# Kernel optimization log

Hardware: AMD Instinct MI355X
Metric: run time of the kernel (lower is better)

## Reference

```python
import jax, jax.numpy as jnp
import numpy as np

N, C = 262144, 128
BN_EPS = 1e-5


def setup_inputs() -> dict:
    key = jax.random.key(0)
    ks = jax.random.split(key, 9)
    s = 1.0 / np.sqrt(C)  # torch Linear default init scale
    return {
        "x": jax.random.normal(ks[0], (N, C), dtype=jnp.float32),
        "W1": jax.random.uniform(ks[1], (C, C), jnp.float32, -s, s),
        "b1": jax.random.uniform(ks[2], (C,), jnp.float32, -s, s),
        "gamma1": jnp.ones((C,), jnp.float32),
        "beta1": jnp.zeros((C,), jnp.float32),
        "W2": jax.random.uniform(ks[3], (C, C), jnp.float32, -s, s),
        "b2": jax.random.uniform(ks[4], (C,), jnp.float32, -s, s),
        "gamma2": jnp.ones((C,), jnp.float32),
        "beta2": jnp.zeros((C,), jnp.float32),
    }


def _batchnorm(h, gamma, beta):
    # training-mode BatchNorm1d: batch mean, biased variance, eps=1e-5
    m = jnp.mean(h, axis=0)
    v = jnp.var(h, axis=0)
    return (h - m) * jax.lax.rsqrt(v + BN_EPS) * gamma + beta


def reference(x, W1, b1, gamma1, beta1, W2, b2, gamma2, beta2):
    res = x
    out = x @ W1.T + b1
    # contextNormalization: only the in-place `d -= mean` loop has effect
    # (return value is discarded in the original), i.e. mean-center over batch
    out = out - jnp.mean(out, axis=0)
    out = jax.nn.relu(_batchnorm(out, gamma1, beta1))
    out = out @ W2.T + b2
    out = out - jnp.mean(out, axis=0)
    out = jax.nn.relu(_batchnorm(out, gamma2, beta2))
    return out + res
```

## Files before the change

### kernel.cpp

```cpp
#include <hip/hip_runtime.h>
#include <hip/hip_bf16.h>

#define NROWS 262144
#define CDIM  128
#define BN_EPS 1e-5f
#define GGRID 1024
#define SPB   (NROWS / 16 / GGRID)

typedef __attribute__((ext_vector_type(8))) short bf16x8;
typedef __attribute__((ext_vector_type(4))) float f32x4;
#define LROW 136

static __device__ __forceinline__ unsigned int f2bf_rtn(float f) {
  unsigned int u = __float_as_uint(f);
  return (u + 0x7fffu + ((u >> 16) & 1u)) >> 16;
}
static __device__ __forceinline__ float bf2f(unsigned int b) {
  return __uint_as_float(b << 16);
}

template <bool NORM>
__global__ void __launch_bounds__(256, 4)
gemm_bn(const float* __restrict__ in, const float* __restrict__ W,
        const float* __restrict__ bias, const float* __restrict__ scsh,
        float* __restrict__ hout, float* __restrict__ stats)
{
  __shared__ __align__(16) short lds[2][2][16][LROW];

  const int tid  = threadIdx.x;
  const int lane = tid & 63;
  const int wave = tid >> 6;
  const int l15  = lane & 15;
  const int lq   = lane >> 4;
  const int wcol = wave * 32;
  const int srow = tid >> 4;
  const int sk0  = (tid & 15) * 8;

  bf16x8 bh[2][4], bl[2][4];
#pragma unroll
  for (int jt = 0; jt < 2; ++jt) {
    const float* wrow = W + (wcol + jt * 16 + l15) * CDIM;
#pragma unroll
    for (int ks = 0; ks < 4; ++ks) {
      const int k0 = ks * 32 + lq * 8;
      f32x4 w0 = *(const f32x4*)(wrow + k0);
      f32x4 w1 = *(const f32x4*)(wrow + k0 + 4);
      float wv[8] = {w0.x,w0.y,w0.z,w0.w,w1.x,w1.y,w1.z,w1.w};
#pragma unroll
      for (int e = 0; e < 8; ++e) {
        unsigned int h = f2bf_rtn(wv[e]);
        bh[jt][ks][e] = (short)h;
        bl[jt][ks][e] = (short)f2bf_rtn(wv[e] - bf2f(h));
      }
    }
  }

  float scv[8], shv[8];
  if constexpr (NORM) {
#pragma unroll
    for (int e = 0; e < 8; ++e) {
      scv[e] = scsh[sk0 + e];
      shv[e] = scsh[CDIM + sk0 + e];
    }
  }

  const float bias0 = bias[wcol + l15];
  const float bias1 = bias[wcol + 16 + l15];
  float s0 = 0.f, s1 = 0.f, q0 = 0.f, q1 = 0.f;

  const int row0 = blockIdx.x * (SPB * 16);

  auto cvt_write = [&](int buf, f32x4 g0, f32x4 g1) {
    float av[8] = {g0.x,g0.y,g0.z,g0.w,g1.x,g1.y,g1.z,g1.w};
    if constexpr (NORM) {
#pragma unroll
      for (int e = 0; e < 8; ++e)
        av[e] = fmaxf(av[e] * scv[e] + shv[e], 0.f);
    }
    bf16x8 hi, lo;
#pragma unroll
    for (int e = 0; e < 8; ++e) {
      unsigned int h = f2bf_rtn(av[e]);
      hi[e] = (short)h;
      lo[e] = (short)f2bf_rtn(av[e] - bf2f(h));
    }
    *(bf16x8*)&lds[buf][0][srow][sk0] = hi;
    *(bf16x8*)&lds[buf][1][srow][sk0] = lo;
  };

  {
    const float* ap = in + (size_t)(row0 + srow) * CDIM + sk0;
    f32x4 g0 = *(const f32x4*)ap;
    f32x4 g1 = *(const f32x4*)(ap + 4);
    cvt_write(0, g0, g1);
  }
  __syncthreads();

  for (int s = 0; s < SPB; ++s) {
    const int cur = s & 1;
    const int r0 = row0 + s * 16;

    f32x4 g0 = {0,0,0,0}, g1 = {0,0,0,0};
    const bool more = (s + 1 < SPB);
    if (more) {
      const float* ap = in + (size_t)(r0 + 16 + srow) * CDIM + sk0;
      g0 = *(const f32x4*)ap;
      g1 = *(const f32x4*)(ap + 4);
    }

    f32x4 acc0 = {0.f,0.f,0.f,0.f};
    f32x4 acc1 = {0.f,0.f,0.f,0.f};
#pragma unroll
    for (int ks = 0; ks < 4; ++ks) {
      const int kc = ks * 32 + lq * 8;
      bf16x8 ah = *(const bf16x8*)&lds[cur][0][l15][kc];
      bf16x8 al = *(const bf16x8*)&lds[cur][1][l15][kc];
      acc0 = __builtin_amdgcn_mfma_f32_16x16x32_bf16(al, bh[0][ks], acc0, 0, 0, 0);
      acc0 = __builtin_amdgcn_mfma_f32_16x16x32_bf16(ah, bl[0][ks], acc0, 0, 0, 0);
      acc0 = __builtin_amdgcn_mfma_f32_16x16x32_bf16(ah, bh[0][ks], acc0, 0, 0, 0);
      acc1 = __builtin_amdgcn_mfma_f32_16x16x32_bf16(al, bh[1][ks], acc1, 0, 0, 0);
      acc1 = __builtin_amdgcn_mfma_f32_16x16x32_bf16(ah, bl[1][ks], acc1, 0, 0, 0);
      acc1 = __builtin_amdgcn_mfma_f32_16x16x32_bf16(ah, bh[1][ks], acc1, 0, 0, 0);
    }

    if (more) cvt_write(cur ^ 1, g0, g1);
    __syncthreads();

    float* op = hout + (size_t)(r0 + lq * 4) * CDIM + wcol + l15;
#pragma unroll
    for (int r = 0; r < 4; ++r) {
      float h0 = acc0[r] + bias0;
      float h1 = acc1[r] + bias1;
      s0 += h0; q0 += h0 * h0;
      s1 += h1; q1 += h1 * h1;
      op[r * CDIM] = h0;
      op[r * CDIM + 16] = h1;
    }
  }

  s0 += __shfl_xor(s0, 16); s0 += __shfl_xor(s0, 32);
  s1 += __shfl_xor(s1, 16); s1 += __shfl_xor(s1, 32);
  q0 += __shfl_xor(q0, 16); q0 += __shfl_xor(q0, 32);
  q1 += __shfl_xor(q1, 16); q1 += __shfl_xor(q1, 32);
  if (lane < 16) {
    atomicAdd(&stats[wcol + lane],             s0);
    atomicAdd(&stats[wcol + 16 + lane],        s1);
    atomicAdd(&stats[CDIM + wcol + lane],      q0);
    atomicAdd(&stats[CDIM + wcol + 16 + lane], q1);
  }
}

__global__ void __launch_bounds__(128)
bn_coeffs(const float* __restrict__ stats, const float* __restrict__ gamma,
          const float* __restrict__ beta, float* __restrict__ scsh)
{
  const int c = threadIdx.x;
  const float inv_n = 1.0f / (float)NROWS;
  float m  = stats[c] * inv_n;
  float v  = stats[CDIM + c] * inv_n - m * m;
  float sc = gamma[c] * rsqrtf(v + BN_EPS);
  scsh[c]        = sc;
  scsh[CDIM + c] = beta[c] - m * sc;
}

__global__ void __launch_bounds__(256)
finalize(const f32x4* __restrict__ h2, const f32x4* __restrict__ xin,
         const float* __restrict__ scsh, f32x4* __restrict__ outp)
{
  const int n4 = NROWS * CDIM / 4;
  const int stride = gridDim.x * blockDim.x * 2;
  for (int i = (blockIdx.x * blockDim.x + threadIdx.x) * 2; i < n4; i += stride) {
    f32x4 hA = h2[i], hB = h2[i + 1];
    f32x4 xA = xin[i], xB = xin[i + 1];
    const int c0 = (i << 2) & (CDIM - 1);
    f32x4 scA = *(const f32x4*)(scsh + c0);
    f32x4 scB = *(const f32x4*)(scsh + c0 + 4);
    f32x4 shA = *(const f32x4*)(scsh + CDIM + c0);
    f32x4 shB = *(const f32x4*)(scsh + CDIM + c0 + 4);
    f32x4 oA, oB;
    oA.x = fmaxf(hA.x * scA.x + shA.x, 0.f) + xA.x;
    oA.y = fmaxf(hA.y * scA.y + shA.y, 0.f) + xA.y;
    oA.z = fmaxf(hA.z * scA.z + shA.z, 0.f) + xA.z;
    oA.w = fmaxf(hA.w * scA.w + shA.w, 0.f) + xA.w;
    oB.x = fmaxf(hB.x * scB.x + shB.x, 0.f) + xB.x;
    oB.y = fmaxf(hB.y * scB.y + shB.y, 0.f) + xB.y;
    oB.z = fmaxf(hB.z * scB.z + shB.z, 0.f) + xB.z;
    oB.w = fmaxf(hB.w * scB.w + shB.w, 0.f) + xB.w;
    __builtin_nontemporal_store(oA, &outp[i]);
    __builtin_nontemporal_store(oB, &outp[i + 1]);
  }
}

extern "C" void kernel_launch(void* const* d_in, const int* in_sizes, int n_in,
                              void* d_out, int out_size, void* d_ws, size_t ws_size,
                              hipStream_t stream) {
  (void)in_sizes; (void)n_in; (void)out_size; (void)ws_size;
  const float* x   = (const float*)d_in[0];
  const float* W1  = (const float*)d_in[1];
  const float* b1  = (const float*)d_in[2];
  const float* g1  = (const float*)d_in[3];
  const float* be1 = (const float*)d_in[4];
  const float* W2  = (const float*)d_in[5];
  const float* b2  = (const float*)d_in[6];
  const float* g2  = (const float*)d_in[7];
  const float* be2 = (const float*)d_in[8];

  float* hbuf   = (float*)d_out;
  float* stats1 = (float*)d_ws;
  float* stats2 = stats1 + 256;
  float* scsh1  = stats1 + 512;
  float* scsh2  = stats1 + 768;

  (void)hipMemsetAsync(d_ws, 0, 2048, stream);

  gemm_bn<false><<<GGRID, 256, 0, stream>>>(x, W1, b1, nullptr, hbuf, stats1);
  bn_coeffs<<<1, 128, 0, stream>>>(stats1, g1, be1, scsh1);
  gemm_bn<true><<<GGRID, 256, 0, stream>>>(hbuf, W2, b2, scsh1, hbuf, stats2);
  bn_coeffs<<<1, 128, 0, stream>>>(stats2, g2, be2, scsh2);
  finalize<<<4096, 256, 0, stream>>>((const f32x4*)hbuf, (const f32x4*)x,
                                     scsh2, (f32x4*)d_out);
}
```

Baseline: 430.1 us.

## Fold BN coefficient kernels into consumers and retune grid and occupancy

Removes the two single-block bn_coeffs launches: each GEMM block and each finalize thread now derives its scale and shift directly from the accumulated stats. The GEMM grid doubles to 2048 blocks and the launch bounds ask for 8 waves per SIMD. Finalize now handles 16 contiguous floats per thread with coefficients kept in registers, and reads x with nontemporal loads. This trades two launch gaps for redundant rsqrt work per thread, and the tighter launch bounds may cause register spills.

Result: slower. 864.7 us (+101.1%).

```diff
diff --git a/kernel.cpp b/kernel.cpp
--- a/kernel.cpp
+++ b/kernel.cpp
@@ -4,7 +4,7 @@
 #define NROWS 262144
 #define CDIM  128
 #define BN_EPS 1e-5f
-#define GGRID 1024
+#define GGRID 2048
 #define SPB   (NROWS / 16 / GGRID)
 
 typedef __attribute__((ext_vector_type(8))) short bf16x8;
@@ -20,9 +20,11 @@
 }
 
 template <bool NORM>
-__global__ void __launch_bounds__(256, 4)
+__global__ void __launch_bounds__(256, 8)
 gemm_bn(const float* __restrict__ in, const float* __restrict__ W,
-        const float* __restrict__ bias, const float* __restrict__ scsh,
+        const float* __restrict__ bias,
+        const float* __restrict__ stats_in,
+        const float* __restrict__ gamma, const float* __restrict__ beta,
         float* __restrict__ hout, float* __restrict__ stats)
 {
   __shared__ __align__(16) short lds[2][2][16][LROW];
@@ -57,10 +59,15 @@
 
   float scv[8], shv[8];
   if constexpr (NORM) {
+    const float inv_n = 1.0f / (float)NROWS;
 #pragma unroll
     for (int e = 0; e < 8; ++e) {
-      scv[e] = scsh[sk0 + e];
-      shv[e] = scsh[CDIM + sk0 + e];
+      const int c = sk0 + e;
+      float m  = stats_in[c] * inv_n;
+      float v  = stats_in[CDIM + c] * inv_n - m * m;
+      float sc = gamma[c] * rsqrtf(v + BN_EPS);
+      scv[e] = sc;
+      shv[e] = beta[c] - m * sc;
     }
   }
 
@@ -150,44 +157,45 @@
   }
 }
 
-__global__ void __launch_bounds__(128)
-bn_coeffs(const float* __restrict__ stats, const float* __restrict__ gamma,
-          const float* __restrict__ beta, float* __restrict__ scsh)
-{
-  const int c = threadIdx.x;
-  const float inv_n = 1.0f / (float)NROWS;
-  float m  = stats[c] * inv_n;
-  float v  = stats[CDIM + c] * inv_n - m * m;
-  float sc = gamma[c] * rsqrtf(v + BN_EPS);
-  scsh[c]        = sc;
-  scsh[CDIM + c] = beta[c] - m * sc;
-}
-
 __global__ void __launch_bounds__(256)
 finalize(const f32x4* __restrict__ h2, const f32x4* __restrict__ xin,
-         const float* __restrict__ scsh, f32x4* __restrict__ outp)
+         const float* __restrict__ stats, const float* __restrict__ gamma,
+         const float* __restrict__ beta, f32x4* __restrict__ outp)
 {
+  const int tid0 = blockIdx.x * blockDim.x + threadIdx.x;
+  const int c0 = (tid0 * 16) & (CDIM - 1);
+
+  const float inv_n = 1.0f / (float)NROWS;
+  float sc[16], sh[16];
+#pragma unroll
+  for (int e = 0; e < 16; ++e) {
+    const int c = c0 + e;
+    float m = stats[c] * inv_n;
+    float v = stats[CDIM + c] * inv_n - m * m;
+    float s = gamma[c] * rsqrtf(v + BN_EPS);
+    sc[e] = s;
+    sh[e] = beta[c] - m * s;
+  }
+
   const int n4 = NROWS * CDIM / 4;
-  const int stride = gridDim.x * blockDim.x * 2;
-  for (int i = (blockIdx.x * blockDim.x + threadIdx.x) * 2; i < n4; i += stride) {
-    f32x4 hA = h2[i], hB = h2[i + 1];
-    f32x4 xA = xin[i], xB = xin[i + 1];
-    const int c0 = (i << 2) & (CDIM - 1);
-    f32x4 scA = *(const f32x4*)(scsh + c0);
-    f32x4 scB = *(const f32x4*)(scsh + c0 + 4);
-    f32x4 shA = *(const f32x4*)(scsh + CDIM + c0);
-    f32x4 shB = *(const f32x4*)(scsh + CDIM + c0 + 4);
-    f32x4 oA, oB;
-    oA.x = fmaxf(hA.x * scA.x + shA.x, 0.f) + xA.x;
-    oA.y = fmaxf(hA.y * scA.y + shA.y, 0.f) + xA.y;
-    oA.z = fmaxf(hA.z * scA.z + shA.z, 0.f) + xA.z;
-    oA.w = fmaxf(hA.w * scA.w + shA.w, 0.f) + xA.w;
-    oB.x = fmaxf(hB.x * scB.x + shB.x, 0.f) + xB.x;
-    oB.y = fmaxf(hB.y * scB.y + shB.y, 0.f) + xB.y;
-    oB.z = fmaxf(hB.z * scB.z + shB.z, 0.f) + xB.z;
-    oB.w = fmaxf(hB.w * scB.w + shB.w, 0.f) + xB.w;
-    __builtin_nontemporal_store(oA, &outp[i]);
-    __builtin_nontemporal_store(oB, &outp[i + 1]);
+  const int stride = gridDim.x * blockDim.x * 4;
+  for (int i = tid0 * 4; i < n4; i += stride) {
+    f32x4 h[4], xv[4], o[4];
+#pragma unroll
+    for (int u = 0; u < 4; ++u) {
+      h[u]  = h2[i + u];
+      xv[u] = __builtin_nontemporal_load(&xin[i + u]);
+    }
+#pragma unroll
+    for (int u = 0; u < 4; ++u) {
+      o[u].x = fmaxf(h[u].x * sc[u*4+0] + sh[u*4+0], 0.f) + xv[u].x;
+      o[u].y = fmaxf(h[u].y * sc[u*4+1] + sh[u*4+1], 0.f) + xv[u].y;
+      o[u].z = fmaxf(h[u].z * sc[u*4+2] + sh[u*4+2], 0.f) + xv[u].z;
+      o[u].w = fmaxf(h[u].w * sc[u*4+3] + sh[u*4+3], 0.f) + xv[u].w;
+    }
+#pragma unroll
+    for (int u = 0; u < 4; ++u)
+      __builtin_nontemporal_store(o[u], &outp[i + u]);
   }
 }
 
@@ -208,15 +216,13 @@
   float* hbuf   = (float*)d_out;
   float* stats1 = (float*)d_ws;
   float* stats2 = stats1 + 256;
-  float* scsh1  = stats1 + 512;
-  float* scsh2  = stats1 + 768;
 
   (void)hipMemsetAsync(d_ws, 0, 2048, stream);
 
-  gemm_bn<false><<<GGRID, 256, 0, stream>>>(x, W1, b1, nullptr, hbuf, stats1);
-  bn_coeffs<<<1, 128, 0, stream>>>(stats1, g1, be1, scsh1);
-  gemm_bn<true><<<GGRID, 256, 0, stream>>>(hbuf, W2, b2, scsh1, hbuf, stats2);
-  bn_coeffs<<<1, 128, 0, stream>>>(stats2, g2, be2, scsh2);
-  finalize<<<4096, 256, 0, stream>>>((const f32x4*)hbuf, (const f32x4*)x,
-                                     scsh2, (f32x4*)d_out);
-}
+  gemm_bn<false><<<GGRID, 256, 0, stream>>>(x, W1, b1, nullptr, nullptr, nullptr,
+                                            hbuf, stats1);
+  gemm_bn<true><<<GGRID, 256, 0, stream>>>(hbuf, W2, b2, stats1, g1, be1,
+                                           hbuf, stats2);
+  finalize<<<2048, 256, 0, stream>>>((const f32x4*)hbuf, (const f32x4*)x,
+                                     stats2, g2, be2, (f32x4*)d_out);
+}
```
